# Optimization experiments

Hardware: AMD Instinct MI355X
Metric: run time of the kernel (lower is better)

The kernel has to match this reference:

```python
import jax, jax.numpy as jnp
import numpy as np

N = 100000      # nodes
E = 1250000     # edges
DIN = 64        # input_dim
H = 64          # hidden_dim
G = 64          # graphs in batch


def setup_inputs() -> dict:
    key = jax.random.key(0)
    ks = jax.random.split(key, 12)
    s = lambda d: 1.0 / np.sqrt(d)  # glorot-ish scale
    return {
        "x": jax.random.normal(ks[0], (N, DIN), dtype=jnp.float32),
        "W1": jax.random.normal(ks[1], (DIN, H), dtype=jnp.float32) * s(DIN),
        "b1": jnp.zeros((H,), jnp.float32),
        "W2": jax.random.normal(ks[2], (H, H), dtype=jnp.float32) * s(H),
        "b2": jnp.zeros((H,), jnp.float32),
        "W3": jax.random.normal(ks[3], (H, H), dtype=jnp.float32) * s(H),
        "b3": jnp.zeros((H,), jnp.float32),
        "Wc1": jax.random.normal(ks[4], (H, H // 2), dtype=jnp.float32) * s(H),
        "bc1": jnp.zeros((H // 2,), jnp.float32),
        "Wc2": jax.random.normal(ks[5], (H // 2, 2), dtype=jnp.float32) * s(H // 2),
        "bc2": jnp.zeros((2,), jnp.float32),
        "edge_index": jax.random.randint(ks[6], (2, E), 0, N, dtype=jnp.int64),
        "batch": jnp.sort(jax.random.randint(ks[7], (N,), 0, G, dtype=jnp.int64)),
    }


def _gcn_norm(edge_index, num_nodes):
    # add self loops, compute symmetric normalization coefficients
    loop = jnp.arange(num_nodes, dtype=edge_index.dtype)
    src = jnp.concatenate([edge_index[0], loop])
    dst = jnp.concatenate([edge_index[1], loop])
    deg = jax.ops.segment_sum(jnp.ones_like(dst, dtype=jnp.float32), dst,
                              num_segments=num_nodes)
    dinv = jnp.where(deg > 0, jax.lax.rsqrt(deg), 0.0)
    norm = dinv[src] * dinv[dst]  # [E+N]
    return src, dst, norm


def _gcn_conv(x, src, dst, norm, W, b, num_nodes):
    h = x @ W                              # [N, out]
    msgs = h[src] * norm[:, None]          # gather + scale, [E+N, out]
    agg = jax.ops.segment_sum(msgs, dst, num_segments=num_nodes)
    return agg + b


def reference(x, W1, b1, W2, b2, W3, b3, Wc1, bc1, Wc2, bc2, edge_index, batch):
    num_nodes = x.shape[0]
    src, dst, norm = _gcn_norm(edge_index, num_nodes)
    h = jax.nn.relu(_gcn_conv(x, src, dst, norm, W1, b1, num_nodes))
    h = jax.nn.relu(_gcn_conv(h, src, dst, norm, W2, b2, num_nodes))
    h = jax.nn.relu(_gcn_conv(h, src, dst, norm, W3, b3, num_nodes))
    # global mean pool over graphs
    sums = jax.ops.segment_sum(h, batch, num_segments=G)          # [G, H]
    cnts = jax.ops.segment_sum(jnp.ones_like(batch, dtype=h.dtype), batch,
                               num_segments=G)
    pooled = sums / jnp.maximum(cnts, 1.0)[:, None]
    # classifier MLP (dropout inactive at inference)
    z = jax.nn.relu(pooled @ Wc1 + bc1)
    return z @ Wc2 + bc2                                          # [G, 2]
```

## Files before the change

kernel.cpp:

```cpp
#include <hip/hip_runtime.h>

constexpr int N = 100000;
constexpr int E = 1250000;
constexpr int G = 64;
constexpr int K = 32;
constexpr int OVF_CAP = 65536;
constexpr int STRIPES = 8;
constexpr int NPS = N / STRIPES;
constexpr int SCAP = 164 * 1024;
constexpr int PR = 1024;
constexpr int PROUNDS = 2;
constexpr int PCHUNK = PR * PROUNDS;
constexpr int PBLKS = (E + PCHUNK - 1) / PCHUNK;
constexpr int SUBN = 391;
constexpr int SUBS = 32;
constexpr int SCAP2 = 6 * 1024;
constexpr int P2CAP = 240;

typedef int v4i __attribute__((ext_vector_type(4)));

__device__ inline unsigned bf16pack(float a, float b) {
  unsigned ua = __float_as_uint(a);
  ua = (ua + 0x7FFF + ((ua >> 16) & 1)) >> 16;
  unsigned ub = __float_as_uint(b);
  ub = (ub + 0x7FFF + ((ub >> 16) & 1)) & 0xFFFF0000u;
  return ua | ub;
}

__global__ void part_kernel(const int* __restrict__ src, const int* __restrict__ dst,
                            unsigned* __restrict__ staged, int* __restrict__ cursors) {
  __shared__ unsigned bins[STRIPES][PR];
  __shared__ int bcnt[STRIPES];
  __shared__ int bbase[STRIPES];
  int tid = threadIdx.x;
  if (tid < STRIPES) bcnt[tid] = 0;
  __syncthreads();
  int base0 = blockIdx.x * PCHUNK;
  auto bin1 = [&](int s, int d) {
    int st = d / NPS;
    unsigned w = ((unsigned)s << 14) | (unsigned)(d - st * NPS);
    int p = atomicAdd(&bcnt[st], 1);
    bins[st][p] = w;
  };
#pragma unroll 1
  for (int r = 0; r < PROUNDS; r++) {
    int base = base0 + r * PR + tid * 4;
    if (base + 3 < E) {
      v4i s4 = __builtin_nontemporal_load((const v4i*)(src + base));
      v4i d4 = __builtin_nontemporal_load((const v4i*)(dst + base));
      bin1(s4.x, d4.x); bin1(s4.y, d4.y); bin1(s4.z, d4.z); bin1(s4.w, d4.w);
    } else {
      for (int j = 0; j < 4; j++)
        if (base + j < E) bin1(src[base + j], dst[base + j]);
    }
    __syncthreads();
    if (tid < STRIPES) bbase[tid] = atomicAdd(&cursors[tid], bcnt[tid]);
    __syncthreads();
#pragma unroll 1
    for (int b = 0; b < STRIPES; b++) {
      int c = bcnt[b];
      unsigned* out = staged + (size_t)b * SCAP + bbase[b];
      for (int k = tid; k < c; k += 256) out[k] = bins[b][k];
    }
    __syncthreads();
    if (tid < STRIPES) bcnt[tid] = 0;
    __syncthreads();
  }
}

__global__ void part2_kernel(const unsigned* __restrict__ staged, const int* __restrict__ cursors,
                             unsigned* __restrict__ staged2, int* __restrict__ cursors2,
                             float* __restrict__ sums) {
  __shared__ unsigned bins[SUBS][P2CAP];
  __shared__ int bcnt[SUBS];
  __shared__ int bbase[SUBS];
  int tid = threadIdx.x;
  if (blockIdx.x == 0) {
    for (int i = tid; i < G * 64 + G; i += 256) sums[i] = 0.f;
  }
  int s = blockIdx.x & (STRIPES - 1);
  int blk = blockIdx.x >> 3;
  if (tid < SUBS) bcnt[tid] = 0;
  __syncthreads();
  int n = cursors[s];
  const unsigned* sbuf = staged + (size_t)s * SCAP;
  int chunk = (n + SUBS - 1) / SUBS;
  int lo2 = blk * chunk, hi2 = min(lo2 + chunk, n);
  for (int i = lo2 + tid; i < hi2; i += 256) {
    unsigned w = __builtin_nontemporal_load(sbuf + i);
    int local = (int)(w & 0x3FFFu);
    int b = local / SUBN;
    int slot = atomicAdd(&bcnt[b], 1);
    if (slot < P2CAP) {
      bins[b][slot] = w;
    } else {
      int q = atomicAdd(&cursors2[s * SUBS + b], 1);
      staged2[(size_t)(s * SUBS + b) * SCAP2 + q] = w;
    }
  }
  __syncthreads();
  if (tid < SUBS) bbase[tid] = atomicAdd(&cursors2[s * SUBS + tid], min(bcnt[tid], P2CAP));
  __syncthreads();
#pragma unroll 1
  for (int b = 0; b < SUBS; b++) {
    int c = min(bcnt[b], P2CAP);
    unsigned* out = staged2 + (size_t)(s * SUBS + b) * SCAP2 + bbase[b];
    for (int k = tid; k < c; k += 256) out[k] = bins[b][k];
  }
}

__global__ __launch_bounds__(512)
void fill_kernel(const unsigned* __restrict__ staged2, const int* __restrict__ cursors2,
                 int* __restrict__ cnt, int* __restrict__ csr,
                 int* __restrict__ ovf, int* __restrict__ ovf_cnt) {
  __shared__ int lcnt[SUBN];
  __shared__ int lcsr[SUBN * K];
  int strp = blockIdx.x & (STRIPES - 1);
  int sub = blockIdx.x >> 3;
  int tid = threadIdx.x;
  for (int i = tid; i < SUBN; i += 512) lcnt[i] = 0;
  __syncthreads();
  int idx2 = strp * SUBS + sub;
  int n2 = cursors2[idx2];
  const unsigned* sbuf = staged2 + (size_t)idx2 * SCAP2;
  int lo = sub * SUBN;
  int nodes = min(SUBN, NPS - lo);
  for (int i = tid; i < n2; i += 512) {
    unsigned w = sbuf[i];
    int local = (int)(w & 0x3FFFu);
    int ld = local - lo;
    int slot = atomicAdd(&lcnt[ld], 1);
    int sr = (int)(w >> 14);
    if (slot < K) {
      lcsr[ld * K + slot] = sr;
    } else {
      int q = atomicAdd(ovf_cnt, 1);
      if (q < OVF_CAP) { ovf[2 * q] = sr; ovf[2 * q + 1] = strp * NPS + local; }
    }
  }
  __syncthreads();
  int nb = strp * NPS + lo;
  for (int i = tid; i < nodes; i += 512) cnt[nb + i] = lcnt[i];
  uint4* dstp = (uint4*)(csr + (size_t)nb * K);
  const uint4* srcp = (const uint4*)lcsr;
  int q4 = nodes * (K / 4);
  for (int i = tid; i < q4; i += 512) dstp[i] = srcp[i];
}

constexpr int XS_STRIDE = 68;
__global__ void gemm_premul_kernel(const float* __restrict__ X, const float* __restrict__ W,
                                   const int* __restrict__ cnt, unsigned* __restrict__ Hs2) {
  __shared__ float Ws[64 * 64];
  __shared__ float Xs[32 * XS_STRIDE];
  int tid = threadIdx.x;
  const float4* W4 = (const float4*)W;
#pragma unroll
  for (int j = 0; j < 4; j++)
    ((float4*)Ws)[tid + j * 256] = W4[tid + j * 256];
  int row0 = blockIdx.x * 32;
  const float4* X4 = (const float4*)(X + row0 * 64);
#pragma unroll
  for (int j = 0; j < 2; j++) {
    int idx = tid + j * 256;
    int r = idx >> 4, q = idx & 15;
    *((float4*)&Xs[r * XS_STRIDE + q * 4]) = X4[idx];
  }
  __syncthreads();
  int r0 = tid >> 4;
  int c = (tid & 15) * 4;
  float4 acc0 = {0, 0, 0, 0}, acc1 = {0, 0, 0, 0};
#pragma unroll
  for (int k = 0; k < 64; k++) {
    float4 w = *((const float4*)&Ws[k * 64 + c]);
    float xa = Xs[r0 * XS_STRIDE + k];
    float xb = Xs[(r0 + 16) * XS_STRIDE + k];
    acc0.x += xa * w.x; acc0.y += xa * w.y; acc0.z += xa * w.z; acc0.w += xa * w.w;
    acc1.x += xb * w.x; acc1.y += xb * w.y; acc1.z += xb * w.z; acc1.w += xb * w.w;
  }
  int ra = row0 + r0, rb = ra + 16;
  float da = rsqrtf((float)cnt[ra] + 1.0f);
  float db = rsqrtf((float)cnt[rb] + 1.0f);
  uint2 pa = make_uint2(bf16pack(acc0.x * da, acc0.y * da), bf16pack(acc0.z * da, acc0.w * da));
  uint2 pb = make_uint2(bf16pack(acc1.x * db, acc1.y * db), bf16pack(acc1.z * db, acc1.w * db));
  ((uint2*)Hs2)[ra * 16 + (tid & 15)] = pa;
  ((uint2*)Hs2)[rb * 16 + (tid & 15)] = pb;
}

template <bool LAST>
__global__ void agg_kernel(const unsigned* __restrict__ Hs2, const int* __restrict__ cnt,
                           const int* __restrict__ csr, const int* __restrict__ ovf,
                           const int* __restrict__ ovf_cnt, const float* __restrict__ b,
                           float* __restrict__ Xout, const int* __restrict__ batch,
                           float* __restrict__ sums, float* __restrict__ cnts) {
  __shared__ float gsum[4][64];
  __shared__ float gcnt[4];
  __shared__ int gmin_s;
  int tid = threadIdx.x;
  if (LAST) {
    if (tid < 256) {
      ((float*)gsum)[tid] = 0.f;
      if (tid < 4) gcnt[tid] = 0.f;
      if (tid == 0) gmin_s = batch[blockIdx.x * 32];
    }
    __syncthreads();
  }
  int lane = tid & 63;
  int i = lane & 7;
  int gb = lane & 56;
  int node = blockIdx.x * 32 + (tid >> 3);
  int c = cnt[node];
  int mg = min(c, K);
  int sv0 = csr[node * K + i];
  int sv1 = csr[node * K + 8 + i];
  int sv2 = csr[node * K + 16 + i];
  int sv3 = csr[node * K + 24 + i];
  int mm = mg;
  mm = max(mm, __shfl_xor(mm, 8));
  mm = max(mm, __shfl_xor(mm, 16));
  mm = max(mm, __shfl_xor(mm, 32));
  const uint4* H4 = (const uint4*)Hs2;
  float acc0 = 0, acc1 = 0, acc2 = 0, acc3 = 0, acc4 = 0, acc5 = 0, acc6 = 0, acc7 = 0;
  auto edge = [&](int sv, int e, int ee) {
    int s = __shfl(sv, gb + ee);
    if (e < mg) {
      uint4 h = H4[s * 8 + i];
      acc0 += __uint_as_float(h.x << 16); acc1 += __uint_as_float(h.x & 0xFFFF0000u);
      acc2 += __uint_as_float(h.y << 16); acc3 += __uint_as_float(h.y & 0xFFFF0000u);
      acc4 += __uint_as_float(h.z << 16); acc5 += __uint_as_float(h.z & 0xFFFF0000u);
      acc6 += __uint_as_float(h.w << 16); acc7 += __uint_as_float(h.w & 0xFFFF0000u);
    }
  };
  if (mm > 0) {
    edge(sv0, 0, 0); edge(sv0, 1, 1); edge(sv0, 2, 2); edge(sv0, 3, 3);
    edge(sv0, 4, 4); edge(sv0, 5, 5); edge(sv0, 6, 6); edge(sv0, 7, 7);
  }
  if (mm > 8) {
    edge(sv1, 8, 0); edge(sv1, 9, 1); edge(sv1, 10, 2); edge(sv1, 11, 3);
    edge(sv1, 12, 4); edge(sv1, 13, 5); edge(sv1, 14, 6); edge(sv1, 15, 7);
  }
  if (mm > 16) {
    edge(sv2, 16, 0); edge(sv2, 17, 1); edge(sv2, 18, 2); edge(sv2, 19, 3);
    edge(sv2, 20, 4); edge(sv2, 21, 5); edge(sv2, 22, 6); edge(sv2, 23, 7);
  }
  if (mm > 24) {
    edge(sv3, 24, 0); edge(sv3, 25, 1); edge(sv3, 26, 2); edge(sv3, 27, 3);
    edge(sv3, 28, 4); edge(sv3, 29, 5); edge(sv3, 30, 6); edge(sv3, 31, 7);
  }
  int on = min(*ovf_cnt, OVF_CAP);
  for (int j = 0; j < on; j++) {
    int dd = ovf[2 * j + 1];
    if (dd == node) {
      uint4 h = H4[ovf[2 * j] * 8 + i];
      acc0 += __uint_as_float(h.x << 16); acc1 += __uint_as_float(h.x & 0xFFFF0000u);
      acc2 += __uint_as_float(h.y << 16); acc3 += __uint_as_float(h.y & 0xFFFF0000u);
      acc4 += __uint_as_float(h.z << 16); acc5 += __uint_as_float(h.z & 0xFFFF0000u);
      acc6 += __uint_as_float(h.w << 16); acc7 += __uint_as_float(h.w & 0xFFFF0000u);
    }
  }
  uint4 hs = H4[node * 8 + i];
  float di = rsqrtf((float)c + 1.0f);
  const float4* b4 = (const float4*)b;
  float4 blo = b4[2 * i], bhi = b4[2 * i + 1];
  float4 o0, o1;
  o0.x = fmaxf(di * (acc0 + __uint_as_float(hs.x << 16)) + blo.x, 0.f);
  o0.y = fmaxf(di * (acc1 + __uint_as_float(hs.x & 0xFFFF0000u)) + blo.y, 0.f);
  o0.z = fmaxf(di * (acc2 + __uint_as_float(hs.y << 16)) + blo.z, 0.f);
  o0.w = fmaxf(di * (acc3 + __uint_as_float(hs.y & 0xFFFF0000u)) + blo.w, 0.f);
  o1.x = fmaxf(di * (acc4 + __uint_as_float(hs.z << 16)) + bhi.x, 0.f);
  o1.y = fmaxf(di * (acc5 + __uint_as_float(hs.z & 0xFFFF0000u)) + bhi.y, 0.f);
  o1.z = fmaxf(di * (acc6 + __uint_as_float(hs.w << 16)) + bhi.z, 0.f);
  o1.w = fmaxf(di * (acc7 + __uint_as_float(hs.w & 0xFFFF0000u)) + bhi.w, 0.f);
  if (!LAST) {
    ((float4*)Xout)[node * 16 + 2 * i] = o0;
    ((float4*)Xout)[node * 16 + 2 * i + 1] = o1;
  } else {
    int g = batch[node];
    int s = g - gmin_s;
    if ((unsigned)s < 4u) {
      atomicAdd(&gsum[s][8 * i + 0], o0.x); atomicAdd(&gsum[s][8 * i + 1], o0.y);
      atomicAdd(&gsum[s][8 * i + 2], o0.z); atomicAdd(&gsum[s][8 * i + 3], o0.w);
      atomicAdd(&gsum[s][8 * i + 4], o1.x); atomicAdd(&gsum[s][8 * i + 5], o1.y);
      atomicAdd(&gsum[s][8 * i + 6], o1.z); atomicAdd(&gsum[s][8 * i + 7], o1.w);
      if (i == 0) atomicAdd(&gcnt[s], 1.f);
    } else {
      atomicAdd(&sums[g * 64 + 8 * i + 0], o0.x); atomicAdd(&sums[g * 64 + 8 * i + 1], o0.y);
      atomicAdd(&sums[g * 64 + 8 * i + 2], o0.z); atomicAdd(&sums[g * 64 + 8 * i + 3], o0.w);
      atomicAdd(&sums[g * 64 + 8 * i + 4], o1.x); atomicAdd(&sums[g * 64 + 8 * i + 5], o1.y);
      atomicAdd(&sums[g * 64 + 8 * i + 6], o1.z); atomicAdd(&sums[g * 64 + 8 * i + 7], o1.w);
      if (i == 0) atomicAdd(&cnts[g], 1.f);
    }
    __syncthreads();
    if (tid < 256) {
      int s2 = tid >> 6, d = tid & 63;
      if (gcnt[s2] > 0.f) {
        atomicAdd(&sums[(gmin_s + s2) * 64 + d], gsum[s2][d]);
        if (d == 0) atomicAdd(&cnts[gmin_s + s2], gcnt[s2]);
      }
    }
  }
}

__global__ void classifier_kernel(const float* __restrict__ sums, const float* __restrict__ cnts,
                                  const float* __restrict__ Wc1, const float* __restrict__ bc1,
                                  const float* __restrict__ Wc2, const float* __restrict__ bc2,
                                  float* __restrict__ out) {
  __shared__ float pooled[64 * 64];
  __shared__ float z[64 * 32];
  int tid = threadIdx.x;
  for (int idx = tid; idx < 64 * 64; idx += 256) {
    int g = idx >> 6;
    pooled[idx] = sums[idx] / fmaxf(cnts[g], 1.0f);
  }
  __syncthreads();
  for (int idx = tid; idx < 64 * 32; idx += 256) {
    int g = idx >> 5, j = idx & 31;
    float acc = bc1[j];
#pragma unroll
    for (int c = 0; c < 64; c++) acc += pooled[g * 64 + c] * Wc1[c * 32 + j];
    z[idx] = fmaxf(acc, 0.f);
  }
  __syncthreads();
  for (int idx = tid; idx < 128; idx += 256) {
    int g = idx >> 1, k = idx & 1;
    float acc = bc2[k];
#pragma unroll
    for (int j = 0; j < 32; j++) acc += z[g * 32 + j] * Wc2[j * 2 + k];
    out[idx] = acc;
  }
}

extern "C" void kernel_launch(void* const* d_in, const int* in_sizes, int n_in,
                              void* d_out, int out_size, void* d_ws, size_t ws_size,
                              hipStream_t stream) {
  const float* x   = (const float*)d_in[0];
  const float* W1  = (const float*)d_in[1];
  const float* b1  = (const float*)d_in[2];
  const float* W2  = (const float*)d_in[3];
  const float* b2  = (const float*)d_in[4];
  const float* W3  = (const float*)d_in[5];
  const float* b3  = (const float*)d_in[6];
  const float* Wc1 = (const float*)d_in[7];
  const float* bc1 = (const float*)d_in[8];
  const float* Wc2 = (const float*)d_in[9];
  const float* bc2 = (const float*)d_in[10];
  const int* ei    = (const int*)d_in[11];
  const int* batch = (const int*)d_in[12];
  const int* src  = ei;
  const int* dstp = ei + E;

  char* ws = (char*)d_ws;
  size_t off = 0;
  auto alloc = [&](size_t bytes) {
    char* p = ws + off;
    off += (bytes + 255) & ~size_t(255);
    return p;
  };
  int*      cnt  = (int*)alloc((size_t)(N + 512) * 4);
  int*      csr  = (int*)alloc((size_t)N * K * 4);
  int*      ovf  = (int*)alloc((size_t)OVF_CAP * 2 * 4);
  unsigned* Hs   = (unsigned*)alloc((size_t)N * 64 * 2);
  float*    B1   = (float*)alloc((size_t)N * 64 * 4);
  float*    sums = (float*)alloc((size_t)(G * 64 + G) * 4);
  float*    cnts = sums + G * 64;
  int*      ovf_cnt  = cnt + N;
  int*      cursors  = cnt + N + 16;
  int*      cursors2 = cnt + N + 64;
  unsigned* staged  = (unsigned*)B1;
  unsigned* staged2 = (unsigned*)B1 + (size_t)STRIPES * SCAP;

  hipMemsetAsync(cnt + N, 0, 512 * 4, stream);

  part_kernel<<<PBLKS, 256, 0, stream>>>(src, dstp, staged, cursors);
  part2_kernel<<<STRIPES * SUBS, 256, 0, stream>>>(staged, cursors, staged2, cursors2, sums);
  fill_kernel<<<STRIPES * SUBS, 512, 0, stream>>>(staged2, cursors2, cnt, csr, ovf, ovf_cnt);

  const float* Xc = x;
  const float* Wl[3] = {W1, W2, W3};
  const float* bl[3] = {b1, b2, b3};
  for (int l = 0; l < 3; l++) {
    gemm_premul_kernel<<<N / 32, 256, 0, stream>>>(Xc, Wl[l], cnt, Hs);
    if (l < 2)
      agg_kernel<false><<<N / 32, 256, 0, stream>>>(Hs, cnt, csr, ovf, ovf_cnt, bl[l], B1,
                                                    batch, sums, cnts);
    else
      agg_kernel<true><<<N / 32, 256, 0, stream>>>(Hs, cnt, csr, ovf, ovf_cnt, bl[l], B1,
                                                   batch, sums, cnts);
    Xc = B1;
  }

  classifier_kernel<<<1, 256, 0, stream>>>(sums, cnts, Wc1, bc1, Wc2, bc2, (float*)d_out);
}
```

Before: 310.3 us.

## Fuse classifier into last aggregation via last-block counter; wave-reduce pooling sums

```diff
diff --git a/kernel.cpp b/kernel.cpp
--- a/kernel.cpp
+++ b/kernel.cpp
@@ -191,12 +191,15 @@
                            const int* __restrict__ csr, const int* __restrict__ ovf,
                            const int* __restrict__ ovf_cnt, const float* __restrict__ b,
                            float* __restrict__ Xout, const int* __restrict__ batch,
-                           float* __restrict__ sums, float* __restrict__ cnts) {
+                           float* __restrict__ sums, float* __restrict__ cnts,
+                           const float* __restrict__ Wc1, const float* __restrict__ bc1,
+                           const float* __restrict__ Wc2, const float* __restrict__ bc2,
+                           float* __restrict__ out, int* __restrict__ done_cnt) {
   __shared__ float gsum[4][64];
   __shared__ float gcnt[4];
   __shared__ int gmin_s;
   int tid = threadIdx.x;
-  if (LAST) {
+  if constexpr (LAST) {
     if (tid < 256) {
       ((float*)gsum)[tid] = 0.f;
       if (tid < 4) gcnt[tid] = 0.f;
@@ -270,24 +273,45 @@
   o1.y = fmaxf(di * (acc5 + __uint_as_float(hs.z & 0xFFFF0000u)) + bhi.y, 0.f);
   o1.z = fmaxf(di * (acc6 + __uint_as_float(hs.w << 16)) + bhi.z, 0.f);
   o1.w = fmaxf(di * (acc7 + __uint_as_float(hs.w & 0xFFFF0000u)) + bhi.w, 0.f);
-  if (!LAST) {
+  if constexpr (!LAST) {
     ((float4*)Xout)[node * 16 + 2 * i] = o0;
     ((float4*)Xout)[node * 16 + 2 * i + 1] = o1;
   } else {
     int g = batch[node];
-    int s = g - gmin_s;
-    if ((unsigned)s < 4u) {
-      atomicAdd(&gsum[s][8 * i + 0], o0.x); atomicAdd(&gsum[s][8 * i + 1], o0.y);
-      atomicAdd(&gsum[s][8 * i + 2], o0.z); atomicAdd(&gsum[s][8 * i + 3], o0.w);
-      atomicAdd(&gsum[s][8 * i + 4], o1.x); atomicAdd(&gsum[s][8 * i + 5], o1.y);
-      atomicAdd(&gsum[s][8 * i + 6], o1.z); atomicAdd(&gsum[s][8 * i + 7], o1.w);
-      if (i == 0) atomicAdd(&gcnt[s], 1.f);
+    int ref = __shfl(g, gb & 0 | i);
+    if (__all(g == ref)) {
+      float v0 = o0.x, v1 = o0.y, v2 = o0.z, v3 = o0.w;
+      float v4 = o1.x, v5 = o1.y, v6 = o1.z, v7 = o1.w;
+#pragma unroll
+      for (int off = 8; off < 64; off <<= 1) {
+        v0 += __shfl_xor(v0, off); v1 += __shfl_xor(v1, off);
+        v2 += __shfl_xor(v2, off); v3 += __shfl_xor(v3, off);
+        v4 += __shfl_xor(v4, off); v5 += __shfl_xor(v5, off);
+        v6 += __shfl_xor(v6, off); v7 += __shfl_xor(v7, off);
+      }
+      if (gb == 0) {
+        int s = ref - gmin_s;
+        atomicAdd(&gsum[s][8 * i + 0], v0); atomicAdd(&gsum[s][8 * i + 1], v1);
+        atomicAdd(&gsum[s][8 * i + 2], v2); atomicAdd(&gsum[s][8 * i + 3], v3);
+        atomicAdd(&gsum[s][8 * i + 4], v4); atomicAdd(&gsum[s][8 * i + 5], v5);
+        atomicAdd(&gsum[s][8 * i + 6], v6); atomicAdd(&gsum[s][8 * i + 7], v7);
+        if (i == 0) atomicAdd(&gcnt[s], 8.f);
+      }
     } else {
-      atomicAdd(&sums[g * 64 + 8 * i + 0], o0.x); atomicAdd(&sums[g * 64 + 8 * i + 1], o0.y);
-      atomicAdd(&sums[g * 64 + 8 * i + 2], o0.z); atomicAdd(&sums[g * 64 + 8 * i + 3], o0.w);
-      atomicAdd(&sums[g * 64 + 8 * i + 4], o1.x); atomicAdd(&sums[g * 64 + 8 * i + 5], o1.y);
-      atomicAdd(&sums[g * 64 + 8 * i + 6], o1.z); atomicAdd(&sums[g * 64 + 8 * i + 7], o1.w);
-      if (i == 0) atomicAdd(&cnts[g], 1.f);
+      int s = g - gmin_s;
+      if ((unsigned)s < 4u) {
+        atomicAdd(&gsum[s][8 * i + 0], o0.x); atomicAdd(&gsum[s][8 * i + 1], o0.y);
+        atomicAdd(&gsum[s][8 * i + 2], o0.z); atomicAdd(&gsum[s][8 * i + 3], o0.w);
+        atomicAdd(&gsum[s][8 * i + 4], o1.x); atomicAdd(&gsum[s][8 * i + 5], o1.y);
+        atomicAdd(&gsum[s][8 * i + 6], o1.z); atomicAdd(&gsum[s][8 * i + 7], o1.w);
+        if (i == 0) atomicAdd(&gcnt[s], 1.f);
+      } else {
+        atomicAdd(&sums[g * 64 + 8 * i + 0], o0.x); atomicAdd(&sums[g * 64 + 8 * i + 1], o0.y);
+        atomicAdd(&sums[g * 64 + 8 * i + 2], o0.z); atomicAdd(&sums[g * 64 + 8 * i + 3], o0.w);
+        atomicAdd(&sums[g * 64 + 8 * i + 4], o1.x); atomicAdd(&sums[g * 64 + 8 * i + 5], o1.y);
+        atomicAdd(&sums[g * 64 + 8 * i + 6], o1.z); atomicAdd(&sums[g * 64 + 8 * i + 7], o1.w);
+        if (i == 0) atomicAdd(&cnts[g], 1.f);
+      }
     }
     __syncthreads();
     if (tid < 256) {
@@ -297,35 +321,36 @@
         if (d == 0) atomicAdd(&cnts[gmin_s + s2], gcnt[s2]);
       }
     }
-  }
-}
-
-__global__ void classifier_kernel(const float* __restrict__ sums, const float* __restrict__ cnts,
-                                  const float* __restrict__ Wc1, const float* __restrict__ bc1,
-                                  const float* __restrict__ Wc2, const float* __restrict__ bc2,
-                                  float* __restrict__ out) {
-  __shared__ float pooled[64 * 64];
-  __shared__ float z[64 * 32];
-  int tid = threadIdx.x;
-  for (int idx = tid; idx < 64 * 64; idx += 256) {
-    int g = idx >> 6;
-    pooled[idx] = sums[idx] / fmaxf(cnts[g], 1.0f);
-  }
-  __syncthreads();
-  for (int idx = tid; idx < 64 * 32; idx += 256) {
-    int g = idx >> 5, j = idx & 31;
-    float acc = bc1[j];
-#pragma unroll
-    for (int c = 0; c < 64; c++) acc += pooled[g * 64 + c] * Wc1[c * 32 + j];
-    z[idx] = fmaxf(acc, 0.f);
-  }
-  __syncthreads();
-  for (int idx = tid; idx < 128; idx += 256) {
-    int g = idx >> 1, k = idx & 1;
-    float acc = bc2[k];
-#pragma unroll
-    for (int j = 0; j < 32; j++) acc += z[g * 32 + j] * Wc2[j * 2 + k];
-    out[idx] = acc;
+    __shared__ int lastflag;
+    __threadfence();
+    __syncthreads();
+    if (tid == 0) lastflag = (atomicAdd(done_cnt, 1) == (int)gridDim.x - 1);
+    __syncthreads();
+    if (lastflag) {
+      __threadfence();
+      __shared__ float pooled[64 * 64];
+      __shared__ float z[64 * 32];
+      for (int idx = tid; idx < 64 * 64; idx += 256) {
+        int gg = idx >> 6;
+        pooled[idx] = sums[idx] / fmaxf(cnts[gg], 1.0f);
+      }
+      __syncthreads();
+      for (int idx = tid; idx < 64 * 32; idx += 256) {
+        int gg = idx >> 5, j = idx & 31;
+        float acc = bc1[j];
+#pragma unroll
+        for (int cc = 0; cc < 64; cc++) acc += pooled[gg * 64 + cc] * Wc1[cc * 32 + j];
+        z[idx] = fmaxf(acc, 0.f);
+      }
+      __syncthreads();
+      for (int idx = tid; idx < 128; idx += 256) {
+        int gg = idx >> 1, k = idx & 1;
+        float acc = bc2[k];
+#pragma unroll
+        for (int j = 0; j < 32; j++) acc += z[gg * 32 + j] * Wc2[j * 2 + k];
+        out[idx] = acc;
+      }
+    }
   }
 }
 
@@ -365,6 +390,7 @@
   int*      ovf_cnt  = cnt + N;
   int*      cursors  = cnt + N + 16;
   int*      cursors2 = cnt + N + 64;
+  int*      done_cnt = cnt + N + 384;
   unsigned* staged  = (unsigned*)B1;
   unsigned* staged2 = (unsigned*)B1 + (size_t)STRIPES * SCAP;
 
@@ -381,12 +407,12 @@
     gemm_premul_kernel<<<N / 32, 256, 0, stream>>>(Xc, Wl[l], cnt, Hs);
     if (l < 2)
       agg_kernel<false><<<N / 32, 256, 0, stream>>>(Hs, cnt, csr, ovf, ovf_cnt, bl[l], B1,
-                                                    batch, sums, cnts);
+                                                    batch, sums, cnts, Wc1, bc1, Wc2, bc2,
+                                                    (float*)d_out, done_cnt);
     else
       agg_kernel<true><<<N / 32, 256, 0, stream>>>(Hs, cnt, csr, ovf, ovf_cnt, bl[l], B1,
-                                                   batch, sums, cnts);
+                                                   batch, sums, cnts, Wc1, bc1, Wc2, bc2,
+                                                   (float*)d_out, done_cnt);
     Xc = B1;
   }
-
-  classifier_kernel<<<1, 256, 0, stream>>>(sums, cnts, Wc1, bc1, Wc2, bc2, (float*)d_out);
-}
+}
```

Result: slower. 503.1 us (+62.1%).
